# Kernel tuning notes

Hardware: AMD Instinct MI355X
Metric: run time of the kernel (lower is better)

## Reference

```python
import math
import jax, jax.numpy as jnp
import numpy as np


def setup_inputs() -> dict:
    key = jax.random.key(0)
    k0, k1, k2 = jax.random.split(key, 3)
    b, c, h, w = 4, 256, 64, 64
    x = jax.random.normal(k0, (b, c, h, w), dtype=jnp.float32)
    # 1x1 conv weights stored as [out_ch, in_ch]
    qkv_w = jax.random.normal(k1, (3 * c, c), dtype=jnp.float32) / math.sqrt(c)
    qkv_b = jnp.zeros((3 * c,), dtype=jnp.float32)
    out_w = jax.random.normal(k2, (c, c), dtype=jnp.float32) / math.sqrt(c)
    out_b = jnp.zeros((c,), dtype=jnp.float32)
    return {"x": x, "qkv_w": qkv_w, "qkv_b": qkv_b, "out_w": out_w, "out_b": out_b}


def reference(x, qkv_w, qkv_b, out_w, out_b):
    b, c, h, w = x.shape
    n = h * w
    # 1x1 conv QKV projection: [b, 3c, h, w]
    qkv = jnp.einsum('oc,bchw->bohw', qkv_w, x) + qkv_b[None, :, None, None]
    # chunk along channels into q, k, v each [b, c, n]
    qkv = qkv.reshape(b, 3, c, n)
    q, k, v = qkv[:, 0], qkv[:, 1], qkv[:, 2]
    # attn[b, i, j] = sum_c k[b,c,i] * q[b,c,j] / sqrt(c); softmax over key axis (dim=-2 -> axis=1)
    scores = jnp.einsum('bcn,bcm->bnm', k, q) / math.sqrt(c)
    attn = jax.nn.softmax(scores, axis=1)
    # out[b, c, j] = sum_i v[b,c,i] * attn[b,i,j]
    o = jnp.einsum('bcn,bnm->bcm', v, attn).reshape(b, c, h, w)
    # output 1x1 conv
    return jnp.einsum('oc,bchw->bohw', out_w, o) + out_b[None, :, None, None]
```

## Files before the change

kernel.cpp:

```cpp
#include <hip/hip_runtime.h>
#include <hip/hip_bf16.h>

typedef unsigned short u16;
typedef unsigned int u32;
typedef __attribute__((ext_vector_type(8))) short short8;
typedef __attribute__((ext_vector_type(4))) short short4v;
typedef __attribute__((ext_vector_type(16))) float f32x16;

#define MFMA32 __builtin_amdgcn_mfma_f32_32x32x16_bf16

#define NSEQ 4096
#define CD 256
#define CF 0.09016844005556021f

__device__ __forceinline__ u16 f2bf(float f) {
  u32 u = __float_as_uint(f);
  u += 0x7fffu + ((u >> 16) & 1u);
  return (u16)(u >> 16);
}
__device__ __forceinline__ float bf2f(short s) {
  return __uint_as_float(((u32)(u16)s) << 16);
}
__device__ __forceinline__ u32 pk2bf(float a, float b) {
  union {
    __hip_bfloat162 h;
    u32 u;
  } cv;
  cv.h = __float22bfloat162_rn(make_float2(a, b));
  return cv.u;
}
__device__ __forceinline__ void async16(const void* g, void* l) {
  __builtin_amdgcn_global_load_lds(
      (const __attribute__((address_space(1))) u32*)g,
      (__attribute__((address_space(3))) u32*)l, 16, 0, 0);
}

__global__ __launch_bounds__(256) void xpose_cast(const float* __restrict__ x,
                                                  u16* __restrict__ x_t,
                                                  const float* __restrict__ qkv_w,
                                                  const float* __restrict__ out_w,
                                                  u16* __restrict__ wq,
                                                  u16* __restrict__ wo) {
  __shared__ float tile[64][65];
  const int t = threadIdx.x;
  {
    int lin = blockIdx.x + 64 * (blockIdx.y + 4 * blockIdx.z);
    int widx = lin * 256 + t;
    if (widx < 768 * CD)
      wq[widx] = f2bf(qkv_w[widx]);
    else
      wo[widx - 768 * CD] = f2bf(out_w[widx - 768 * CD]);
  }
  const int b = blockIdx.z;
  const int n0 = blockIdx.x * 64, c0 = blockIdx.y * 64;
  const float* xb = x + (size_t)b * CD * NSEQ;
  const int cr = t >> 4, nc4 = (t & 15) * 4;
#pragma unroll
  for (int i = 0; i < 4; ++i) {
    int c = cr + 16 * i;
    float4 v = *(const float4*)(xb + (size_t)(c0 + c) * NSEQ + n0 + nc4);
    tile[c][nc4 + 0] = v.x;
    tile[c][nc4 + 1] = v.y;
    tile[c][nc4 + 2] = v.z;
    tile[c][nc4 + 3] = v.w;
  }
  __syncthreads();
  const int n = t & 63, cc = (t >> 6) * 16;
  u16* dst = x_t + (size_t)b * NSEQ * CD + (size_t)(n0 + n) * CD + c0 + cc;
#pragma unroll
  for (int j = 0; j < 4; ++j) {
    short4v pv;
#pragma unroll
    for (int r = 0; r < 4; ++r) pv[r] = (short)f2bf(tile[cc + 4 * j + r][n]);
    *(short4v*)(dst + 4 * j) = pv;
  }
}

__global__ __launch_bounds__(512, 1) void qkv_gemm3(
    const u16* __restrict__ wq, const float* __restrict__ qkv_b,
    const u16* __restrict__ x_t, u16* __restrict__ q_t, u16* __restrict__ k_t,
    u16* __restrict__ v_) {
  __shared__ u16 __align__(16) Wls[128 * 256];
  __shared__ u16 __align__(16) Bls[128 * 256];
  const int t = threadIdx.x, w = t >> 6, lane = t & 63;
  const int l31 = lane & 31, l5 = lane >> 5;
  const int os = w & 3, nh = w >> 2;
  const int n0 = blockIdx.x * 128, o0 = blockIdx.y * 128, b = blockIdx.z;
  const u16* Xb = x_t + (size_t)b * NSEQ * CD;
#pragma unroll
  for (int j = 0; j < 8; ++j) {
    int r = w * 16 + j * 2 + l5;
    async16(wq + (size_t)(o0 + r) * CD + ((l31 ^ (r & 7)) * 8),
            Wls + (w * 16 + j * 2) * 256);
    async16(Xb + (size_t)(n0 + r) * CD + ((l31 ^ (r & 7)) * 8),
            Bls + (w * 16 + j * 2) * 256);
  }
  __builtin_amdgcn_s_waitcnt(0);
  __syncthreads();
  f32x16 acc0, acc1;
#pragma unroll
  for (int i = 0; i < 16; ++i) {
    acc0[i] = 0.f;
    acc1[i] = 0.f;
  }
  const int ra = os * 32 + l31;
  const int rb0 = nh * 64 + l31, rb1 = rb0 + 32;
#pragma unroll
  for (int kc = 0; kc < 16; ++kc) {
    short8 a = *(const short8*)(Wls + ra * 256 + (((kc * 2 + l5) ^ (ra & 7)) * 8));
    short8 b0 = *(const short8*)(Bls + rb0 * 256 + (((kc * 2 + l5) ^ (rb0 & 7)) * 8));
    short8 b1 = *(const short8*)(Bls + rb1 * 256 + (((kc * 2 + l5) ^ (rb1 & 7)) * 8));
    acc0 = MFMA32(a, b0, acc0, 0, 0, 0);
    acc1 = MFMA32(a, b1, acc1, 0, 0, 0);
  }
  const int otype = blockIdx.y >> 1;
  const int obase = o0 + os * 32;
#pragma unroll
  for (int na = 0; na < 2; ++na) {
    f32x16& acc = na ? acc1 : acc0;
    const int n_g = n0 + nh * 64 + na * 32 + l31;
    if (otype < 2) {
      u16* dst = (otype == 0 ? q_t : k_t) + (size_t)b * NSEQ * CD +
                 (size_t)n_g * CD + (obase - otype * 256);
#pragma unroll
      for (int g = 0; g < 4; ++g) {
        float4 bv = *(const float4*)(qkv_b + obase + g * 8 + l5 * 4);
        const float* bp = (const float*)&bv;
        short4v pk;
#pragma unroll
        for (int r = 0; r < 4; ++r) pk[r] = (short)f2bf(acc[g * 4 + r] + bp[r]);
        *(short4v*)(dst + g * 8 + l5 * 4) = pk;
      }
    } else {
      u16* dst = v_ + (size_t)b * CD * NSEQ;
#pragma unroll
      for (int g = 0; g < 4; ++g) {
        float4 bv = *(const float4*)(qkv_b + obase + g * 8 + l5 * 4);
        const float* bp = (const float*)&bv;
#pragma unroll
        for (int r = 0; r < 4; ++r) {
          int c = obase - 512 + g * 8 + l5 * 4 + r;
          dst[(size_t)c * NSEQ + n_g] = f2bf(acc[g * 4 + r] + bp[r]);
        }
      }
    }
  }
}

__global__ __launch_bounds__(256, 2) void flash8(const u16* __restrict__ q_t,
                                                 const u16* __restrict__ k_t,
                                                 const u16* __restrict__ v_,
                                                 u16* __restrict__ opart,
                                                 float2* __restrict__ ml) {
  __shared__ u16 __align__(16) Kls[2][32 * 256];
  __shared__ u16 __align__(16) Vls[2][128 * 64];

  const int t = threadIdx.x, w = t >> 6, lane = t & 63;
  const int l31 = lane & 31, l5 = lane >> 5;

  const int linear = blockIdx.x;
  const int xcd = linear & 7, slot = linear >> 3;
  const int b = xcd >> 1;
  const int q = (xcd & 1) * 2 + (slot >> 5);
  const int mblk = slot & 31;
  const int m0 = mblk * 128;
  const int nbase = q * 1024;

  const u16* Qb = q_t + (size_t)b * NSEQ * CD;
  const u16* Kb = k_t + (size_t)b * NSEQ * CD;
  const u16* Vb = v_ + (size_t)b * CD * NSEQ;

  const int mrow = m0 + w * 32 + l31;

  short8 qf[16];
#pragma unroll
  for (int kc = 0; kc < 16; ++kc)
    qf[kc] = *(const short8*)(Qb + (size_t)mrow * CD + kc * 16 + l5 * 8);

  int krow[4];
  const u16* ksrc[4];
#pragma unroll
  for (int j = 0; j < 4; ++j) {
    krow[j] = w * 8 + j * 2 + l5;
    ksrc[j] = Kb + (size_t)krow[j] * CD + ((l31 ^ (krow[j] & 7)) * 8);
  }
  const u16* vsrc[4];
#pragma unroll
  for (int j = 0; j < 4; ++j) {
    int c2 = w * 32 + j * 8 + (lane >> 3);
    int chl = (lane & 7) ^ (c2 & 7);
    int c = (c2 << 1) | (chl >> 2);
    vsrc[j] = Vb + (size_t)c * NSEQ + (chl & 3) * 8;
  }

#pragma unroll
  for (int j = 0; j < 4; ++j) {
    async16(ksrc[j] + (size_t)nbase * CD, &Kls[0][(w * 8 + j * 2) * 256]);
    async16(vsrc[j] + nbase, &Vls[0][(w * 32 + j * 8) * 64]);
  }

  float mst = -3.0e38f, lst = 0.f;
  f32x16 oa[8];
#pragma unroll
  for (int i = 0; i < 8; ++i)
#pragma unroll
    for (int r = 0; r < 16; ++r) oa[i][r] = 0.f;

  for (int tt = 0; tt < 32; ++tt) {
    const int cur = tt & 1;
    __builtin_amdgcn_s_waitcnt(0);
    __syncthreads();
    if (tt + 1 < 32) {
      const int n0 = nbase + (tt + 1) * 32;
      const int nxt = cur ^ 1;
#pragma unroll
      for (int j = 0; j < 4; ++j) {
        async16(ksrc[j] + (size_t)n0 * CD, &Kls[nxt][(w * 8 + j * 2) * 256]);
        async16(vsrc[j] + n0, &Vls[nxt][(w * 32 + j * 8) * 64]);
      }
    }
    f32x16 sa;
#pragma unroll
    for (int i = 0; i < 16; ++i) sa[i] = 0.f;
#pragma unroll
    for (int kc = 0; kc < 16; ++kc) {
      short8 a =
          *(const short8*)(&Kls[cur][l31 * 256 + (((kc * 2 + l5) ^ (l31 & 7)) * 8)]);
      sa = MFMA32(a, qf[kc], sa, 0, 0, 0);
    }
    float rm = sa[0];
#pragma unroll
    for (int i = 1; i < 16; ++i) rm = fmaxf(rm, sa[i]);
    rm = fmaxf(rm, __shfl_xor(rm, 32));
    float mnew = fmaxf(mst, rm * CF);
    float al = exp2f(mst - mnew);
    mst = mnew;
    u32 d[4][2];
    float ls = 0.f;
#pragma unroll
    for (int gg = 0; gg < 4; ++gg) {
      float p0 = exp2f(sa[gg * 4 + 0] * CF - mnew);
      float p1 = exp2f(sa[gg * 4 + 1] * CF - mnew);
      float p2 = exp2f(sa[gg * 4 + 2] * CF - mnew);
      float p3 = exp2f(sa[gg * 4 + 3] * CF - mnew);
      ls += (p0 + p1) + (p2 + p3);
      d[gg][0] = pk2bf(p0, p1);
      d[gg][1] = pk2bf(p2, p3);
    }
    ls += __shfl_xor(ls, 32);
    lst = lst * al + ls;
    if (__ballot(al != 1.0f)) {
#pragma unroll
      for (int i = 0; i < 8; ++i)
#pragma unroll
        for (int r = 0; r < 16; ++r) oa[i][r] *= al;
    }
    short8 pf[2];
#pragma unroll
    for (int f = 0; f < 2; ++f) {
      const int g0 = f * 2;
      u32 sx0 = l5 ? d[g0][0] : d[g0 + 1][0];
      u32 sx1 = l5 ? d[g0][1] : d[g0 + 1][1];
      u32 e0 = (u32)__shfl_xor((int)sx0, 32);
      u32 e1 = (u32)__shfl_xor((int)sx1, 32);
      union {
        u32 u[4];
        short8 s8;
      } cv;
      cv.u[0] = l5 ? e0 : d[g0][0];
      cv.u[1] = l5 ? e1 : d[g0][1];
      cv.u[2] = l5 ? d[g0 + 1][0] : e0;
      cv.u[3] = l5 ? d[g0 + 1][1] : e1;
      pf[f] = cv.s8;
    }
#pragma unroll
    for (int f = 0; f < 2; ++f) {
#pragma unroll
      for (int ct = 0; ct < 8; ++ct) {
        int c2r = ct * 16 + (l31 >> 1);
        int chl = ((l31 & 1) << 2) | (f * 2 + l5);
        short8 vf =
            *(const short8*)(&Vls[cur][c2r * 64 + ((chl ^ (c2r & 7)) * 8)]);
        oa[ct] = MFMA32(vf, pf[f], oa[ct], 0, 0, 0);
      }
    }
  }

  float inv = 1.0f / lst;
  u16* dst = opart + ((size_t)(q * 4 + b) * NSEQ + mrow) * CD;
#pragma unroll
  for (int ct = 0; ct < 8; ++ct)
#pragma unroll
    for (int gg = 0; gg < 4; ++gg) {
      short4v pk;
#pragma unroll
      for (int r = 0; r < 4; ++r) pk[r] = (short)f2bf(oa[ct][gg * 4 + r] * inv);
      *(short4v*)(dst + ct * 32 + gg * 8 + l5 * 4) = pk;
    }
  if (lane < 32)
    ml[(size_t)(q * 4 + b) * NSEQ + mrow] = make_float2(mst, lst);
}

__global__ __launch_bounds__(512, 1) void out_gemm6(
    const u16* __restrict__ wo, const float* __restrict__ out_b,
    const u16* __restrict__ opart, const float2* __restrict__ ml,
    float* __restrict__ out) {
  __shared__ u16 __align__(16) Wls[128 * 256];
  __shared__ u16 __align__(16) Bls[128 * 256];
  const int t = threadIdx.x, w = t >> 6, lane = t & 63;
  const int l31 = lane & 31, l5 = lane >> 5;
  const int os = w & 3, nh = w >> 2;
  const int n0 = blockIdx.x * 128, o0 = blockIdx.y * 128, b = blockIdx.z;
#pragma unroll
  for (int j = 0; j < 8; ++j) {
    int r = w * 16 + j * 2 + l5;
    async16(wo + (size_t)(o0 + r) * CD + ((l31 ^ (r & 7)) * 8),
            Wls + (w * 16 + j * 2) * 256);
  }
#pragma unroll
  for (int i = 0; i < 8; ++i) {
    int idx = i * 512 + t;
    int r = idx >> 5, p = idx & 31;
    int n = n0 + r;
    float2 st[4];
#pragma unroll
    for (int qq = 0; qq < 4; ++qq) st[qq] = ml[(size_t)(qq * 4 + b) * NSEQ + n];
    float M = fmaxf(fmaxf(st[0].x, st[1].x), fmaxf(st[2].x, st[3].x));
    float wt[4], tot = 0.f;
#pragma unroll
    for (int qq = 0; qq < 4; ++qq) {
      wt[qq] = st[qq].y * exp2f(st[qq].x - M);
      tot += wt[qq];
    }
    float inv = 1.0f / tot;
    float acc[8] = {};
#pragma unroll
    for (int qq = 0; qq < 4; ++qq) {
      float wq_ = wt[qq] * inv;
      short8 xq =
          *(const short8*)(opart + ((size_t)(qq * 4 + b) * NSEQ + n) * CD + p * 8);
#pragma unroll
      for (int e = 0; e < 8; ++e) acc[e] += wq_ * bf2f(xq[e]);
    }
    short8 om;
#pragma unroll
    for (int e = 0; e < 8; ++e) om[e] = (short)f2bf(acc[e]);
    *(short8*)(Bls + r * 256 + ((p ^ (r & 7)) * 8)) = om;
  }
  __builtin_amdgcn_s_waitcnt(0);
  __syncthreads();
  f32x16 acc0, acc1;
#pragma unroll
  for (int i = 0; i < 16; ++i) {
    acc0[i] = 0.f;
    acc1[i] = 0.f;
  }
  const int ra = os * 32 + l31;
  const int rb0 = nh * 64 + l31, rb1 = rb0 + 32;
#pragma unroll
  for (int kc = 0; kc < 16; ++kc) {
    short8 a = *(const short8*)(Wls + ra * 256 + (((kc * 2 + l5) ^ (ra & 7)) * 8));
    short8 b0 = *(const short8*)(Bls + rb0 * 256 + (((kc * 2 + l5) ^ (rb0 & 7)) * 8));
    short8 b1 = *(const short8*)(Bls + rb1 * 256 + (((kc * 2 + l5) ^ (rb1 & 7)) * 8));
    acc0 = MFMA32(a, b0, acc0, 0, 0, 0);
    acc1 = MFMA32(a, b1, acc1, 0, 0, 0);
  }
  const int obase = o0 + os * 32;
#pragma unroll
  for (int na = 0; na < 2; ++na) {
    f32x16& acc = na ? acc1 : acc0;
    const int n_g = n0 + nh * 64 + na * 32 + l31;
#pragma unroll
    for (int g = 0; g < 4; ++g) {
      float4 bv = *(const float4*)(out_b + obase + g * 8 + l5 * 4);
      const float* bp = (const float*)&bv;
#pragma unroll
      for (int r = 0; r < 4; ++r) {
        int o = obase + g * 8 + l5 * 4 + r;
        out[((size_t)b * CD + o) * NSEQ + n_g] = acc[g * 4 + r] + bp[r];
      }
    }
  }
}

extern "C" void kernel_launch(void* const* d_in, const int* in_sizes, int n_in,
                              void* d_out, int out_size, void* d_ws,
                              size_t ws_size, hipStream_t stream) {
  const float* x = (const float*)d_in[0];
  const float* qkv_w = (const float*)d_in[1];
  const float* qkv_b = (const float*)d_in[2];
  const float* out_w = (const float*)d_in[3];
  const float* out_b = (const float*)d_in[4];
  float* out = (float*)d_out;

  const size_t SZ = (size_t)4 * NSEQ * CD;
  u16* x_t = (u16*)d_ws;
  u16* q_t = x_t + SZ;
  u16* k_t = q_t + SZ;
  u16* v_ = k_t + SZ;
  u16* opart = v_ + SZ;
  u16* wq = opart + 4 * SZ;
  u16* wo = wq + 768 * CD;
  float2* ml = (float2*)(wo + CD * CD);

  xpose_cast<<<dim3(64, 4, 4), dim3(256), 0, stream>>>(x, x_t, qkv_w, out_w,
                                                       wq, wo);
  qkv_gemm3<<<dim3(32, 6, 4), dim3(512), 0, stream>>>(wq, qkv_b, x_t, q_t, k_t,
                                                      v_);
  flash8<<<dim3(512), dim3(256), 0, stream>>>(q_t, k_t, v_, opart, ml);
  out_gemm6<<<dim3(32, 2, 4), dim3(512), 0, stream>>>(wo, out_b, opart, ml,
                                                      out);
}
```

Baseline: 205.5 us.

## Switch flash kernel to 16x16x32 MFMA with 8 waves of 16 query rows

Rewrites the attention kernel so each of 8 waves owns 16 query rows and uses 16x16x32 bf16 MFMAs instead of 32x32x16, with the block size doubled to 512 threads and the K/V tile loads split across more waves. This halves per-wave accumulator and Q-fragment register use, which should allow more waves in flight to hide LDS and softmax latency. It also adds s_setprio around the MFMA sections and a two-stage shuffle to rearrange P into B-operand layout. In exchange there are more K LDS reads per MFMA and extra cross-lane shuffles per tile.

```diff
diff --git a/kernel.cpp b/kernel.cpp
--- a/kernel.cpp
+++ b/kernel.cpp
@@ -6,8 +6,10 @@
 typedef __attribute__((ext_vector_type(8))) short short8;
 typedef __attribute__((ext_vector_type(4))) short short4v;
 typedef __attribute__((ext_vector_type(16))) float f32x16;
+typedef __attribute__((ext_vector_type(4))) float f32x4;
 
 #define MFMA32 __builtin_amdgcn_mfma_f32_32x32x16_bf16
+#define MFMA16 __builtin_amdgcn_mfma_f32_16x16x32_bf16
 
 #define NSEQ 4096
 #define CD 256
@@ -147,7 +149,7 @@
   }
 }
 
-__global__ __launch_bounds__(256, 2) void flash8(const u16* __restrict__ q_t,
+__global__ __launch_bounds__(512, 4) void flash9(const u16* __restrict__ q_t,
                                                  const u16* __restrict__ k_t,
                                                  const u16* __restrict__ v_,
                                                  u16* __restrict__ opart,
@@ -157,6 +159,7 @@
 
   const int t = threadIdx.x, w = t >> 6, lane = t & 63;
   const int l31 = lane & 31, l5 = lane >> 5;
+  const int l15 = lane & 15, g = lane >> 4;
 
   const int linear = blockIdx.x;
   const int xcd = linear & 7, slot = linear >> 3;
@@ -170,41 +173,44 @@
   const u16* Kb = k_t + (size_t)b * NSEQ * CD;
   const u16* Vb = v_ + (size_t)b * CD * NSEQ;
 
-  const int mrow = m0 + w * 32 + l31;
-
-  short8 qf[16];
-#pragma unroll
-  for (int kc = 0; kc < 16; ++kc)
-    qf[kc] = *(const short8*)(Qb + (size_t)mrow * CD + kc * 16 + l5 * 8);
-
-  int krow[4];
-  const u16* ksrc[4];
-#pragma unroll
-  for (int j = 0; j < 4; ++j) {
-    krow[j] = w * 8 + j * 2 + l5;
-    ksrc[j] = Kb + (size_t)krow[j] * CD + ((l31 ^ (krow[j] & 7)) * 8);
-  }
-  const u16* vsrc[4];
-#pragma unroll
-  for (int j = 0; j < 4; ++j) {
-    int c2 = w * 32 + j * 8 + (lane >> 3);
+  const int mrow = m0 + w * 16 + l15;
+
+  short8 qf[8];
+#pragma unroll
+  for (int kk = 0; kk < 8; ++kk)
+    qf[kk] = *(const short8*)(Qb + (size_t)mrow * CD + kk * 32 + g * 8);
+
+  const u16* ksrc[2];
+#pragma unroll
+  for (int j = 0; j < 2; ++j) {
+    int kr = w * 4 + j * 2 + l5;
+    ksrc[j] = Kb + (size_t)kr * CD + ((l31 ^ (kr & 7)) * 8);
+  }
+  const u16* vsrc[2];
+#pragma unroll
+  for (int j = 0; j < 2; ++j) {
+    int c2 = w * 16 + j * 8 + (lane >> 3);
     int chl = (lane & 7) ^ (c2 & 7);
     int c = (c2 << 1) | (chl >> 2);
     vsrc[j] = Vb + (size_t)c * NSEQ + (chl & 3) * 8;
   }
 
 #pragma unroll
-  for (int j = 0; j < 4; ++j) {
-    async16(ksrc[j] + (size_t)nbase * CD, &Kls[0][(w * 8 + j * 2) * 256]);
-    async16(vsrc[j] + nbase, &Vls[0][(w * 32 + j * 8) * 64]);
+  for (int j = 0; j < 2; ++j) {
+    async16(ksrc[j] + (size_t)nbase * CD, &Kls[0][(w * 4 + j * 2) * 256]);
+    async16(vsrc[j] + nbase, &Vls[0][(w * 16 + j * 8) * 64]);
   }
 
   float mst = -3.0e38f, lst = 0.f;
-  f32x16 oa[8];
-#pragma unroll
-  for (int i = 0; i < 8; ++i)
-#pragma unroll
-    for (int r = 0; r < 16; ++r) oa[i][r] = 0.f;
+  f32x4 oa[16];
+#pragma unroll
+  for (int i = 0; i < 16; ++i)
+#pragma unroll
+    for (int r = 0; r < 4; ++r) oa[i][r] = 0.f;
+
+  const int vbase =
+      (l15 >> 1) * 64 + (((((l15 & 1) << 2) | g) ^ ((l15 >> 1) & 7)) * 8);
+  const int kx = l15 & 7;
 
   for (int tt = 0; tt < 32; ++tt) {
     const int cur = tt & 1;
@@ -214,90 +220,93 @@
       const int n0 = nbase + (tt + 1) * 32;
       const int nxt = cur ^ 1;
 #pragma unroll
-      for (int j = 0; j < 4; ++j) {
-        async16(ksrc[j] + (size_t)n0 * CD, &Kls[nxt][(w * 8 + j * 2) * 256]);
-        async16(vsrc[j] + n0, &Vls[nxt][(w * 32 + j * 8) * 64]);
+      for (int j = 0; j < 2; ++j) {
+        async16(ksrc[j] + (size_t)n0 * CD, &Kls[nxt][(w * 4 + j * 2) * 256]);
+        async16(vsrc[j] + n0, &Vls[nxt][(w * 16 + j * 8) * 64]);
       }
     }
-    f32x16 sa;
-#pragma unroll
-    for (int i = 0; i < 16; ++i) sa[i] = 0.f;
-#pragma unroll
-    for (int kc = 0; kc < 16; ++kc) {
-      short8 a =
-          *(const short8*)(&Kls[cur][l31 * 256 + (((kc * 2 + l5) ^ (l31 & 7)) * 8)]);
-      sa = MFMA32(a, qf[kc], sa, 0, 0, 0);
-    }
-    float rm = sa[0];
-#pragma unroll
-    for (int i = 1; i < 16; ++i) rm = fmaxf(rm, sa[i]);
+    f32x4 sa0, sa1;
+#pragma unroll
+    for (int r = 0; r < 4; ++r) {
+      sa0[r] = 0.f;
+      sa1[r] = 0.f;
+    }
+    __builtin_amdgcn_s_setprio(1);
+#pragma unroll
+    for (int kk = 0; kk < 8; ++kk) {
+      const int ch = kk * 4 + g;
+      short8 a0 = *(const short8*)(&Kls[cur][l15 * 256 + ((ch ^ kx) * 8)]);
+      short8 a1 =
+          *(const short8*)(&Kls[cur][(16 + l15) * 256 + ((ch ^ kx) * 8)]);
+      sa0 = MFMA16(a0, qf[kk], sa0, 0, 0, 0);
+      sa1 = MFMA16(a1, qf[kk], sa1, 0, 0, 0);
+    }
+    __builtin_amdgcn_s_setprio(0);
+    float rm = fmaxf(fmaxf(fmaxf(sa0[0], sa0[1]), fmaxf(sa0[2], sa0[3])),
+                     fmaxf(fmaxf(sa1[0], sa1[1]), fmaxf(sa1[2], sa1[3])));
+    rm = fmaxf(rm, __shfl_xor(rm, 16));
     rm = fmaxf(rm, __shfl_xor(rm, 32));
     float mnew = fmaxf(mst, rm * CF);
     float al = exp2f(mst - mnew);
     mst = mnew;
-    u32 d[4][2];
-    float ls = 0.f;
-#pragma unroll
-    for (int gg = 0; gg < 4; ++gg) {
-      float p0 = exp2f(sa[gg * 4 + 0] * CF - mnew);
-      float p1 = exp2f(sa[gg * 4 + 1] * CF - mnew);
-      float p2 = exp2f(sa[gg * 4 + 2] * CF - mnew);
-      float p3 = exp2f(sa[gg * 4 + 3] * CF - mnew);
-      ls += (p0 + p1) + (p2 + p3);
-      d[gg][0] = pk2bf(p0, p1);
-      d[gg][1] = pk2bf(p2, p3);
-    }
+    float p00 = exp2f(sa0[0] * CF - mnew), p01 = exp2f(sa0[1] * CF - mnew);
+    float p02 = exp2f(sa0[2] * CF - mnew), p03 = exp2f(sa0[3] * CF - mnew);
+    float p10 = exp2f(sa1[0] * CF - mnew), p11 = exp2f(sa1[1] * CF - mnew);
+    float p12 = exp2f(sa1[2] * CF - mnew), p13 = exp2f(sa1[3] * CF - mnew);
+    float ls = ((p00 + p01) + (p02 + p03)) + ((p10 + p11) + (p12 + p13));
+    ls += __shfl_xor(ls, 16);
     ls += __shfl_xor(ls, 32);
     lst = lst * al + ls;
     if (__ballot(al != 1.0f)) {
 #pragma unroll
-      for (int i = 0; i < 8; ++i)
-#pragma unroll
-        for (int r = 0; r < 16; ++r) oa[i][r] *= al;
-    }
-    short8 pf[2];
-#pragma unroll
-    for (int f = 0; f < 2; ++f) {
-      const int g0 = f * 2;
-      u32 sx0 = l5 ? d[g0][0] : d[g0 + 1][0];
-      u32 sx1 = l5 ? d[g0][1] : d[g0 + 1][1];
-      u32 e0 = (u32)__shfl_xor((int)sx0, 32);
-      u32 e1 = (u32)__shfl_xor((int)sx1, 32);
-      union {
-        u32 u[4];
-        short8 s8;
-      } cv;
-      cv.u[0] = l5 ? e0 : d[g0][0];
-      cv.u[1] = l5 ? e1 : d[g0][1];
-      cv.u[2] = l5 ? d[g0 + 1][0] : e0;
-      cv.u[3] = l5 ? d[g0 + 1][1] : e1;
-      pf[f] = cv.s8;
-    }
-#pragma unroll
-    for (int f = 0; f < 2; ++f) {
-#pragma unroll
-      for (int ct = 0; ct < 8; ++ct) {
-        int c2r = ct * 16 + (l31 >> 1);
-        int chl = ((l31 & 1) << 2) | (f * 2 + l5);
-        short8 vf =
-            *(const short8*)(&Vls[cur][c2r * 64 + ((chl ^ (c2r & 7)) * 8)]);
-        oa[ct] = MFMA32(vf, pf[f], oa[ct], 0, 0, 0);
-      }
-    }
+      for (int i = 0; i < 16; ++i)
+#pragma unroll
+        for (int r = 0; r < 4; ++r) oa[i][r] *= al;
+    }
+    u32 A0 = pk2bf(p00, p01), A1 = pk2bf(p02, p03);
+    u32 B0 = pk2bf(p10, p11), B1 = pk2bf(p12, p13);
+    const int g0 = g & 1, h = g >> 1;
+    u32 ea0 = (u32)__shfl_xor((int)A0, 16), ea1 = (u32)__shfl_xor((int)A1, 16);
+    u32 eb0 = (u32)__shfl_xor((int)B0, 16), eb1 = (u32)__shfl_xor((int)B1, 16);
+    u32 CA0 = g0 ? ea0 : A0, CA1 = g0 ? ea1 : A1;
+    u32 CA2 = g0 ? A0 : ea0, CA3 = g0 ? A1 : ea1;
+    u32 CB0 = g0 ? eb0 : B0, CB1 = g0 ? eb1 : B1;
+    u32 CB2 = g0 ? B0 : eb0, CB3 = g0 ? B1 : eb1;
+    u32 s0 = h ? CA0 : CB0, s1 = h ? CA1 : CB1;
+    u32 s2 = h ? CA2 : CB2, s3 = h ? CA3 : CB3;
+    u32 r0 = (u32)__shfl_xor((int)s0, 32), r1 = (u32)__shfl_xor((int)s1, 32);
+    u32 r2 = (u32)__shfl_xor((int)s2, 32), r3 = (u32)__shfl_xor((int)s3, 32);
+    u32 k0 = h ? CB0 : CA0, k1 = h ? CB1 : CA1;
+    u32 k2 = h ? CB2 : CA2, k3 = h ? CB3 : CA3;
+    const bool own = (g0 == h);
+    union {
+      u32 u[4];
+      short8 s8;
+    } pfv;
+    pfv.u[0] = own ? k0 : r0;
+    pfv.u[1] = own ? k1 : r1;
+    pfv.u[2] = own ? k2 : r2;
+    pfv.u[3] = own ? k3 : r3;
+    short8 pf = pfv.s8;
+    __builtin_amdgcn_s_setprio(1);
+#pragma unroll
+    for (int ct = 0; ct < 16; ++ct) {
+      short8 vf = *(const short8*)(&Vls[cur][ct * 512 + vbase]);
+      oa[ct] = MFMA16(vf, pf, oa[ct], 0, 0, 0);
+    }
+    __builtin_amdgcn_s_setprio(0);
   }
 
   float inv = 1.0f / lst;
   u16* dst = opart + ((size_t)(q * 4 + b) * NSEQ + mrow) * CD;
 #pragma unroll
-  for (int ct = 0; ct < 8; ++ct)
-#pragma unroll
-    for (int gg = 0; gg < 4; ++gg) {
-      short4v pk;
-#pragma unroll
-      for (int r = 0; r < 4; ++r) pk[r] = (short)f2bf(oa[ct][gg * 4 + r] * inv);
-      *(short4v*)(dst + ct * 32 + gg * 8 + l5 * 4) = pk;
-    }
-  if (lane < 32)
+  for (int ct = 0; ct < 16; ++ct) {
+    short4v pk;
+#pragma unroll
+    for (int r = 0; r < 4; ++r) pk[r] = (short)f2bf(oa[ct][r] * inv);
+    *(short4v*)(dst + ct * 16 + g * 4) = pk;
+  }
+  if (lane < 16)
     ml[(size_t)(q * 4 + b) * NSEQ + mrow] = make_float2(mst, lst);
 }
 
@@ -407,7 +416,7 @@
                                                        wq, wo);
   qkv_gemm3<<<dim3(32, 6, 4), dim3(512), 0, stream>>>(wq, qkv_b, x_t, q_t, k_t,
                                                       v_);
-  flash8<<<dim3(512), dim3(256), 0, stream>>>(q_t, k_t, v_, opart, ml);
+  flash9<<<dim3(512), dim3(512), 0, stream>>>(q_t, k_t, v_, opart, ml);
   out_gemm6<<<dim3(32, 2, 4), dim3(512), 0, stream>>>(wo, out_b, opart, ml,
                                                       out);
 }
```

Result: slower. 223.9 us (+9.0%).
